# Kernel optimization log

Measured on AMD Instinct MI355X. Metric: run time of the kernel, lower is better.

The kernel has to match this reference:

```python
import jax, jax.numpy as jnp
import numpy as np

B, Q, DIM, HEADS, RPE_H, HGRID, WGRID, STRIDE = 2, 900, 256, 8, 512, 64, 64, 16
KV = HGRID * WGRID


def setup_inputs() -> dict:
    key = jax.random.key(0)
    ks = jax.random.split(key, 16)
    s = 0.02
    return {
        "hidden_states": jax.random.normal(ks[0], (B, Q, DIM), jnp.float32),
        "reference_points": jax.random.uniform(ks[1], (B, Q, 1, 4), jnp.float32),
        "key_value_states": jax.random.normal(ks[2], (B, KV, DIM), jnp.float32),
        "spatial_shapes": jnp.array([[HGRID, WGRID]], dtype=jnp.int64),
        "attention_mask": jax.random.randint(ks[3], (B, KV), 0, 2, jnp.int32),
        "mlp1_w1": jax.random.normal(ks[4], (RPE_H, 2), jnp.float32) * s,
        "mlp1_b1": jnp.zeros((RPE_H,), jnp.float32),
        "mlp1_w2": jax.random.normal(ks[5], (HEADS, RPE_H), jnp.float32) * s,
        "mlp2_w1": jax.random.normal(ks[6], (RPE_H, 2), jnp.float32) * s,
        "mlp2_b1": jnp.zeros((RPE_H,), jnp.float32),
        "mlp2_w2": jax.random.normal(ks[7], (HEADS, RPE_H), jnp.float32) * s,
        "q_w": jax.random.normal(ks[8], (DIM, DIM), jnp.float32) * s,
        "q_b": jnp.zeros((DIM,), jnp.float32),
        "k_w": jax.random.normal(ks[9], (DIM, DIM), jnp.float32) * s,
        "k_b": jnp.zeros((DIM,), jnp.float32),
        "v_w": jax.random.normal(ks[10], (DIM, DIM), jnp.float32) * s,
        "v_b": jnp.zeros((DIM,), jnp.float32),
        "o_w": jax.random.normal(ks[11], (DIM, DIM), jnp.float32) * s,
        "o_b": jnp.zeros((DIM,), jnp.float32),
    }


def _attn(hidden_states, reference_points, key_value_states, h, w, attention_mask,
          mlp1_w1, mlp1_b1, mlp1_w2, mlp2_w1, mlp2_b1, mlp2_w2,
          q_w, q_b, k_w, k_b, v_w, v_b, o_w, o_b):
    b, q_len, dim = hidden_states.shape
    nh = mlp1_w2.shape[0]
    hd = dim // nh
    scale = hd ** -0.5
    stride = STRIDE

    # boxes cxcywh -> x1y1x2y2, scaled to absolute pixel coords (reparam=False)
    c, sz = reference_points[..., :2], reference_points[..., 2:]
    ref = jnp.concatenate([c - sz / 2, c + sz / 2], axis=-1)  # (B,Q,1,4)
    mult = jnp.array([w * stride, h * stride, w * stride, h * stride], dtype=ref.dtype)
    ref = ref * mult

    pos_x = (jnp.arange(w, dtype=jnp.float32) + 0.5) * stride
    pos_y = (jnp.arange(h, dtype=jnp.float32) + 0.5) * stride
    dx = ref[..., 0::2] - pos_x[None, None, :, None]  # (B,Q,W,2)
    dy = ref[..., 1::2] - pos_y[None, None, :, None]  # (B,Q,H,2)

    # small MLPs: 2 -> rpe_hidden -> num_heads
    rpe_x = jax.nn.relu(dx @ mlp1_w1.T + mlp1_b1) @ mlp1_w2.T  # (B,Q,W,nh)
    rpe_y = jax.nn.relu(dy @ mlp2_w1.T + mlp2_b1) @ mlp2_w2.T  # (B,Q,H,nh)
    rpe = rpe_x[:, :, None, :, :] + rpe_y[:, :, :, None, :]    # (B,Q,H,W,nh)
    rpe = rpe.reshape(b, q_len, h * w, nh).transpose(0, 3, 1, 2)  # (B,nh,Q,K)

    queries = (hidden_states @ q_w.T + q_b).reshape(b, q_len, nh, hd).transpose(0, 2, 1, 3) * scale
    kv_len = key_value_states.shape[1]
    keys = (key_value_states @ k_w.T + k_b).reshape(b, kv_len, nh, hd).transpose(0, 2, 1, 3)
    values = (key_value_states @ v_w.T + v_b).reshape(b, kv_len, nh, hd).transpose(0, 2, 1, 3)

    scores = jnp.einsum('bhqd,bhkd->bhqk', queries, keys) + rpe
    scores = scores + attention_mask.astype(scores.dtype)[:, None, None] * (-100.0)
    probs = jax.nn.softmax(scores, axis=-1)
    ctx = jnp.einsum('bhqk,bhkd->bhqd', probs, values)
    ctx = ctx.transpose(0, 2, 1, 3).reshape(b, q_len, dim)
    return ctx @ o_w.T + o_b


def reference(hidden_states, reference_points, key_value_states, spatial_shapes, attention_mask,
              mlp1_w1, mlp1_b1, mlp1_w2, mlp2_w1, mlp2_b1, mlp2_w2,
              q_w, q_b, k_w, k_b, v_w, v_b, o_w, o_b):
    h = int(spatial_shapes[0, 0])
    w = int(spatial_shapes[0, 1])
    return _attn(hidden_states, reference_points, key_value_states, h, w, attention_mask,
                 mlp1_w1, mlp1_b1, mlp1_w2, mlp2_w1, mlp2_b1, mlp2_w2,
                 q_w, q_b, k_w, k_b, v_w, v_b, o_w, o_b)
```

## Files before the change

### kernel.cpp

```cpp
#include <hip/hip_runtime.h>
#include <math.h>

#define NB    2
#define NQ    900
#define NQP   960
#define NKV   4096
#define DIMM  256
#define NHEAD 8
#define HD    32
#define RPEH  512
#define GRID  64
#define SPLIT 4
#define KVSEG 1024
#define NT    16

typedef short short8 __attribute__((ext_vector_type(8)));
typedef float f32x4 __attribute__((ext_vector_type(4)));
typedef unsigned uint2v __attribute__((ext_vector_type(2)));
typedef unsigned short u16;
typedef unsigned short u16x4 __attribute__((ext_vector_type(4)));

__device__ inline u16 f2bf(float f) {
    unsigned u = __builtin_bit_cast(unsigned, f);
    u += 0x7fff + ((u >> 16) & 1);
    return (u16)(u >> 16);
}
__device__ inline unsigned packbf2(float a, float b) {
    unsigned ua = __builtin_bit_cast(unsigned, a);
    ua += 0x7fff + ((ua >> 16) & 1);
    unsigned ub = __builtin_bit_cast(unsigned, b);
    ub += 0x7fff + ((ub >> 16) & 1);
    return (ua >> 16) | (ub & 0xffff0000u);
}

#define HS4  115200
#define KV4  524288
#define W4   16384
__global__ __launch_bounds__(256) void conv_bf16(
    const float* __restrict__ hs, const float* __restrict__ kv,
    const float* __restrict__ qw, const float* __restrict__ kw,
    const float* __restrict__ vw,
    u16* __restrict__ hsbf, u16* __restrict__ kvbf,
    u16* __restrict__ qwbf, u16* __restrict__ kwbf, u16* __restrict__ vwbf)
{
    const int total = HS4 + KV4 + 3 * W4;
    for (int g = blockIdx.x * 256 + threadIdx.x; g < total; g += gridDim.x * 256) {
        const float* s; u16* d; int off;
        if (g < HS4)                       { s = hs; d = hsbf; off = g; }
        else if (g < HS4 + KV4)            { s = kv; d = kvbf; off = g - HS4; }
        else if (g < HS4 + KV4 + W4)       { s = qw; d = qwbf; off = g - HS4 - KV4; }
        else if (g < HS4 + KV4 + 2 * W4)   { s = kw; d = kwbf; off = g - HS4 - KV4 - W4; }
        else                               { s = vw; d = vwbf; off = g - HS4 - KV4 - 2 * W4; }
        f32x4 v = *(const f32x4*)(s + (size_t)off * 4);
        *(u16x4*)(d + (size_t)off * 4) =
            (u16x4){f2bf(v[0]), f2bf(v[1]), f2bf(v[2]), f2bf(v[3])};
    }
}

__global__ __launch_bounds__(256) void proj_mfma(
    const u16* __restrict__ A,
    const u16* __restrict__ W0, const float* __restrict__ B0,
    const u16* __restrict__ W1, const float* __restrict__ B1,
    u16* __restrict__ outRow, u16* __restrict__ outVt,
    int M, float scale)
{
    __shared__ u16 Abuf[2][4096];
    __shared__ u16 Bbuf[2][4096];

    const u16* W = W0; const float* bias = B0; bool vt = false;
    if (blockIdx.z == 1) { W = W1; bias = B1; vt = true; }

    const int t    = threadIdx.x;
    const int lane = t & 63;
    const int w    = t >> 6;
    const int wm   = w >> 1, wn = w & 1;
    const int m0   = blockIdx.x * 128;
    const int n0   = blockIdx.y * 128;

    const int r0 = t >> 2, c0 = t & 3;
    const int r1 = r0 + 64;
    const int s0 = r0 * 4 + (c0 ^ (r0 & 3));
    const int s1 = r1 * 4 + (c0 ^ (r1 & 3));
    const u16* Arow0 = A + (size_t)(m0 + r0) * DIMM + c0 * 8;
    const u16* Arow1 = A + (size_t)(m0 + r1) * DIMM + c0 * 8;
    const u16* Wrow0 = W + (size_t)(n0 + r0) * DIMM + c0 * 8;
    const u16* Wrow1 = W + (size_t)(n0 + r1) * DIMM + c0 * 8;

    const int fr = lane & 15, fkc = lane >> 4;
    int aslot[4], bslot[4];
    #pragma unroll
    for (int f = 0; f < 4; ++f) {
        int ar = wm * 64 + f * 16 + fr;
        int br = wn * 64 + f * 16 + fr;
        aslot[f] = ar * 4 + (fkc ^ (ar & 3));
        bslot[f] = br * 4 + (fkc ^ (br & 3));
    }
    float bv[4];
    #pragma unroll
    for (int f = 0; f < 4; ++f) bv[f] = bias[n0 + wn * 64 + f * 16 + fr];

    f32x4 acc[4][4] = {};

    {
        short8 a0 = *(const short8*)(Arow0);
        short8 a1 = *(const short8*)(Arow1);
        short8 b0 = *(const short8*)(Wrow0);
        short8 b1 = *(const short8*)(Wrow1);
        *(short8*)&Abuf[0][s0 * 8] = a0;
        *(short8*)&Abuf[0][s1 * 8] = a1;
        *(short8*)&Bbuf[0][s0 * 8] = b0;
        *(short8*)&Bbuf[0][s1 * 8] = b1;
    }
    __syncthreads();

    int cur = 0;
    for (int kt = 0; kt < 8; ++kt) {
        short8 na0, na1, nb0, nb1;
        if (kt < 7) {
            int ko = (kt + 1) * 32;
            na0 = *(const short8*)(Arow0 + ko);
            na1 = *(const short8*)(Arow1 + ko);
            nb0 = *(const short8*)(Wrow0 + ko);
            nb1 = *(const short8*)(Wrow1 + ko);
        }
        short8 af[4], bf[4];
        #pragma unroll
        for (int f = 0; f < 4; ++f) {
            af[f] = *(const short8*)&Abuf[cur][aslot[f] * 8];
            bf[f] = *(const short8*)&Bbuf[cur][bslot[f] * 8];
        }
        #pragma unroll
        for (int i = 0; i < 4; ++i)
            #pragma unroll
            for (int j = 0; j < 4; ++j)
                acc[i][j] = __builtin_amdgcn_mfma_f32_16x16x32_bf16(af[i], bf[j], acc[i][j], 0, 0, 0);
        if (kt < 7) {
            *(short8*)&Abuf[cur ^ 1][s0 * 8] = na0;
            *(short8*)&Abuf[cur ^ 1][s1 * 8] = na1;
            *(short8*)&Bbuf[cur ^ 1][s0 * 8] = nb0;
            *(short8*)&Bbuf[cur ^ 1][s1 * 8] = nb1;
        }
        __syncthreads();
        cur ^= 1;
    }

    #pragma unroll
    for (int i = 0; i < 4; ++i) {
        int mbase = m0 + wm * 64 + i * 16 + 4 * fkc;
        #pragma unroll
        for (int j = 0; j < 4; ++j) {
            int n = n0 + wn * 64 + j * 16 + fr;
            #pragma unroll
            for (int r = 0; r < 4; ++r) {
                int gm = mbase + r;
                if (gm < M) {
                    float v = (acc[i][j][r] + bv[j]) * scale;
                    if (!vt) {
                        outRow[(size_t)gm * DIMM + n] = f2bf(v);
                    } else {
                        int bb = gm >> 12, kvi = gm & 4095;
                        int hh = n >> 5, dd = n & 31;
                        outVt[(size_t)((bb * NHEAD + hh) * HD + dd) * NKV + kvi] = f2bf(v);
                    }
                }
            }
        }
    }
}

__global__ __launch_bounds__(256) void rpe_kernel(
    const float* __restrict__ ref_pts,
    const float* __restrict__ w1x, const float* __restrict__ b1x,
    const float* __restrict__ w2x,
    const float* __restrict__ w1y, const float* __restrict__ b1y,
    const float* __restrict__ w2y,
    float* __restrict__ rpex, float* __restrict__ rpey)
{
    __shared__ f32x4 wpk[RPEH];
    __shared__ float w2t[RPEH][NHEAD];
    __shared__ float2 red[3][4][4][64];

    const int t   = threadIdx.x;
    const int m   = blockIdx.x & 1;
    const int bq0 = (blockIdx.x >> 1) * 4;

    const float* w1 = m ? w1y : w1x;
    const float* b1 = m ? b1y : b1x;
    const float* w2 = m ? w2y : w2x;
    for (int r = t; r < RPEH; r += 256) {
        float a = w1[r * 2], b = w1[r * 2 + 1];
        wpk[r] = (f32x4){a, b, b1[r], a + b};
    }
    for (int i = t; i < RPEH * NHEAD; i += 256) {
        int h = i >> 9, r = i & 511;
        w2t[r][h] = w2[h * RPEH + r];
    }
    __syncthreads();

    const int lane = t & 63;
    const int wv   = t >> 6;
    const float p  = (lane + 0.5f) * 16.f;

    float lo[4], hi[4];
    #pragma unroll
    for (int j = 0; j < 4; ++j) {
        const float* q = ref_pts + (size_t)(bq0 + j) * 4;
        float c = m ? q[1] : q[0];
        float s = m ? q[3] : q[2];
        lo[j] = (c - s * 0.5f) * 1024.f;
        hi[j] = (c + s * 0.5f) * 1024.f;
    }

    float2 acc[4][4] = {};
    const int r0 = wv * 128;
    #pragma unroll 4
    for (int rr = 0; rr < 128; ++rr) {
        int r = r0 + rr;
        f32x4 W  = wpk[r];
        f32x4 u0 = *(const f32x4*)&w2t[r][0];
        f32x4 u1 = *(const f32x4*)&w2t[r][4];
        float bp = W[3] * p;
        #pragma unroll
        for (int tk = 0; tk < 4; ++tk) {
            float al  = W[0] * lo[tk] + W[1] * hi[tk] + W[2];
            float hid = fmaxf(al - bp, 0.f);
            acc[tk][0].x += u0[0] * hid;  acc[tk][0].y += u0[1] * hid;
            acc[tk][1].x += u0[2] * hid;  acc[tk][1].y += u0[3] * hid;
            acc[tk][2].x += u1[0] * hid;  acc[tk][2].y += u1[1] * hid;
            acc[tk][3].x += u1[2] * hid;  acc[tk][3].y += u1[3] * hid;
        }
    }

    if (wv > 0) {
        #pragma unroll
        for (int tk = 0; tk < 4; ++tk)
            #pragma unroll
            for (int j = 0; j < 4; ++j)
                red[wv - 1][tk][j][lane] = acc[tk][j];
    }
    __syncthreads();
    if (wv == 0) {
        float* outp = m ? rpey : rpex;
        #pragma unroll
        for (int tk = 0; tk < 4; ++tk) {
            size_t base = (size_t)(bq0 + tk) * (NHEAD * GRID) + lane;
            #pragma unroll
            for (int j = 0; j < 4; ++j) {
                float2 s0 = red[0][tk][j][lane];
                float2 s1 = red[1][tk][j][lane];
                float2 s2 = red[2][tk][j][lane];
                float sx = acc[tk][j].x + s0.x + s1.x + s2.x;
                float sy = acc[tk][j].y + s0.y + s1.y + s2.y;
                outp[base + (2 * j) * GRID]     = sx;
                outp[base + (2 * j + 1) * GRID] = sy;
            }
        }
    }
}

__global__ __launch_bounds__(256) void attn_mfma(
    const u16* __restrict__ Qbf, const u16* __restrict__ Kbf,
    const u16* __restrict__ Vt,
    const float* __restrict__ RX, const float* __restrict__ RY,
    const int* __restrict__ mask,
    float* __restrict__ pctx, float2* __restrict__ pml)
{
    __shared__ short8 kbuf[2][4][64];
    __shared__ short8 vbuf[2][4][64];
    __shared__ unsigned pbuf[4][2][64][4];
    __shared__ float ry_s[16][68];
    __shared__ float mbuf[2][64];

    const int tid  = threadIdx.x;
    const int lane = tid & 63;
    const int w    = tid >> 6;
    const int q15  = lane & 15;
    const int g    = lane >> 4;
    const int qt = blockIdx.x, h = blockIdx.y;
    const int b  = blockIdx.z >> 2;
    const int sp = blockIdx.z & 3;
    const int q0 = qt * 64;
    const int wq = w * 16 + q15;
    const int gq = q0 + wq;
    const bool qok = gq < NQ;
    const int kv0g = sp * KVSEG;

    float rxr[16];
    {
        const float* rxrow = RX + (size_t)(b * NQ + (qok ? gq : 0)) * (NHEAD * GRID) + h * GRID;
        #pragma unroll
        for (int kt = 0; kt < 4; ++kt)
            #pragma unroll
            for (int r = 0; r < 4; ++r)
                rxr[kt * 4 + r] = qok ? rxrow[16 * kt + 4 * g + r] : 0.f;
    }
    for (int idx = tid; idx < 16 * 64; idx += 256) {
        int y = idx & 15, q = idx >> 4;
        int gq2 = q0 + q;
        ry_s[y][q] = (gq2 < NQ)
            ? RY[(size_t)(b * NQ + gq2) * (NHEAD * GRID) + h * GRID + sp * 16 + y] : 0.f;
    }

    short8 qf = *(const short8*)(Qbf + ((size_t)(b * NQ + gq)) * DIMM + h * HD + 8 * g);

    const int sr = tid >> 2, sc = tid & 3;
    const int vd = tid >> 3, vc = tid & 7;
    const size_t kbase = ((size_t)(b * NKV + kv0g + sr)) * DIMM + h * HD + 8 * sc;
    const size_t vbase = ((size_t)((b * NHEAD + h) * HD + vd)) * NKV + kv0g + 8 * vc;

    kbuf[0][sr >> 4][(sr & 15) + 16 * sc] = *(const short8*)(Kbf + kbase);
    vbuf[0][(vc >> 2) * 2 + (vd >> 4)][16 * (vc & 3) + (vd & 15)] = *(const short8*)(Vt + vbase);
    if (tid < 64) mbuf[0][tid] = -100.f * (float)mask[b * NKV + kv0g + tid];
    __syncthreads();

    f32x4 cacc0 = {0.f, 0.f, 0.f, 0.f};
    f32x4 cacc1 = {0.f, 0.f, 0.f, 0.f};
    float m_run = -1e30f, l_run = 0.f;
    int cur = 0;

    for (int t = 0; t < NT; ++t) {
        short8 rk = {}, rv = {};
        float rm = 0.f;
        if (t < NT - 1) {
            size_t kvn = (size_t)(t + 1) * 64;
            rk = *(const short8*)(Kbf + kbase + kvn * DIMM);
            rv = *(const short8*)(Vt + vbase + kvn);
            if (tid < 64) rm = -100.f * (float)mask[b * NKV + kv0g + kvn + tid];
        }

        f32x4 zero = {0.f, 0.f, 0.f, 0.f};
        f32x4 s[4];
        __builtin_amdgcn_s_setprio(1);
        #pragma unroll
        for (int kt = 0; kt < 4; ++kt)
            s[kt] = __builtin_amdgcn_mfma_f32_16x16x32_bf16(kbuf[cur][kt][lane], qf, zero, 0, 0, 0);
        __builtin_amdgcn_s_setprio(0);

        float ryb = ry_s[t][wq];
        #pragma unroll
        for (int kt = 0; kt < 4; ++kt) {
            #pragma unroll
            for (int r = 0; r < 4; ++r)
                s[kt][r] += rxr[kt * 4 + r] + ryb + mbuf[cur][16 * kt + 4 * g + r];
        }

        float mloc = s[0][0];
        #pragma unroll
        for (int kt = 0; kt < 4; ++kt)
            #pragma unroll
            for (int r = 0; r < 4; ++r) mloc = fmaxf(mloc, s[kt][r]);
        mloc = fmaxf(mloc, __shfl_xor(mloc, 16));
        mloc = fmaxf(mloc, __shfl_xor(mloc, 32));
        float mnew = fmaxf(m_run, mloc);
        float fsc  = __expf(m_run - mnew);
        float psum = 0.f;
        #pragma unroll
        for (int kt = 0; kt < 4; ++kt)
            #pragma unroll
            for (int r = 0; r < 4; ++r) {
                float pv = __expf(s[kt][r] - mnew);
                s[kt][r] = pv;
                psum += pv;
            }
        psum += __shfl_xor(psum, 16);
        psum += __shfl_xor(psum, 32);
        l_run = l_run * fsc + psum;
        m_run = mnew;
        cacc0 *= fsc;
        cacc1 *= fsc;

        #pragma unroll
        for (int kt = 0; kt < 4; ++kt) {
            unsigned d0 = packbf2(s[kt][0], s[kt][1]);
            unsigned d1 = packbf2(s[kt][2], s[kt][3]);
            int lt = 16 * ((2 * kt + (g >> 1)) & 3) + q15;
            uint2v* dst = (uint2v*)&pbuf[w][kt >> 1][lt][2 * (g & 1)];
            *dst = (uint2v){d0, d1};
        }

        __builtin_amdgcn_s_setprio(1);
        #pragma unroll
        for (int sk = 0; sk < 2; ++sk) {
            short8 pf = *(const short8*)&pbuf[w][sk][lane][0];
            cacc0 = __builtin_amdgcn_mfma_f32_16x16x32_bf16(vbuf[cur][sk * 2 + 0][lane], pf, cacc0, 0, 0, 0);
            cacc1 = __builtin_amdgcn_mfma_f32_16x16x32_bf16(vbuf[cur][sk * 2 + 1][lane], pf, cacc1, 0, 0, 0);
        }
        __builtin_amdgcn_s_setprio(0);

        if (t < NT - 1) {
            kbuf[cur ^ 1][sr >> 4][(sr & 15) + 16 * sc] = rk;
            vbuf[cur ^ 1][(vc >> 2) * 2 + (vd >> 4)][16 * (vc & 3) + (vd & 15)] = rv;
            if (tid < 64) mbuf[cur ^ 1][tid] = rm;
        }
        __syncthreads();
        cur ^= 1;
    }

    size_t prow = (size_t)(sp * NB + b) * NQP + gq;
    float* pc = pctx + prow * DIMM + h * HD;
    #pragma unroll
    for (int r = 0; r < 4; ++r) {
        pc[4 * g + r]      = cacc0[r];
        pc[16 + 4 * g + r] = cacc1[r];
    }
    if (g == 0) {
        float2 v; v.x = m_run; v.y = l_run;
        pml[prow * NHEAD + h] = v;
    }
}

__global__ __launch_bounds__(256) void attn_reduce(
    const float* __restrict__ pctx, const float2* __restrict__ pml,
    float* __restrict__ CTX)
{
    const int bq = blockIdx.x;
    const int b = bq / NQ, q = bq - b * NQ;
    const int c = threadIdx.x;
    const int h = c >> 5;

    float m[SPLIT], l[SPLIT];
    #pragma unroll
    for (int sp = 0; sp < SPLIT; ++sp) {
        float2 v = pml[((size_t)(sp * NB + b) * NQP + q) * NHEAD + h];
        m[sp] = v.x; l[sp] = v.y;
    }
    float ms = fmaxf(fmaxf(m[0], m[1]), fmaxf(m[2], m[3]));
    float L = 0.f, acc = 0.f;
    #pragma unroll
    for (int sp = 0; sp < SPLIT; ++sp) {
        float wgt = __expf(m[sp] - ms);
        L   += wgt * l[sp];
        acc += wgt * pctx[((size_t)(sp * NB + b) * NQP + q) * DIMM + c];
    }
    CTX[(size_t)bq * DIMM + c] = acc / L;
}

__global__ __launch_bounds__(256) void gemm_bias_f32(
    const float* __restrict__ A, const float* __restrict__ W,
    const float* __restrict__ bias, float* __restrict__ C,
    int M, int N, int K)
{
    __shared__ float As[32][33];
    __shared__ float Ws[32][33];
    const int t  = threadIdx.x;
    const int tr = t >> 4;
    const int tc = t & 15;
    const int brow = blockIdx.y * 32;
    const int bcol = blockIdx.x * 32;
    float acc00 = 0.f, acc01 = 0.f, acc10 = 0.f, acc11 = 0.f;

    for (int kt = 0; kt < K; kt += 32) {
        #pragma unroll
        for (int i = 0; i < 4; ++i) {
            int idx = t + i * 256;
            int r = idx >> 5, c = idx & 31;
            int gr = brow + r;
            As[r][c] = (gr < M) ? A[(size_t)gr * K + kt + c] : 0.f;
            Ws[r][c] = W[(size_t)(bcol + r) * K + kt + c];
        }
        __syncthreads();
        #pragma unroll 8
        for (int k = 0; k < 32; ++k) {
            float a0 = As[tr * 2][k], a1 = As[tr * 2 + 1][k];
            float w0 = Ws[tc * 2][k], w1 = Ws[tc * 2 + 1][k];
            acc00 += a0 * w0; acc01 += a0 * w1;
            acc10 += a1 * w0; acc11 += a1 * w1;
        }
        __syncthreads();
    }
    int gc0 = bcol + tc * 2, gc1 = gc0 + 1;
    int gr0 = brow + tr * 2, gr1 = gr0 + 1;
    if (gr0 < M) {
        C[(size_t)gr0 * N + gc0] = acc00 + bias[gc0];
        C[(size_t)gr0 * N + gc1] = acc01 + bias[gc1];
    }
    if (gr1 < M) {
        C[(size_t)gr1 * N + gc0] = acc10 + bias[gc0];
        C[(size_t)gr1 * N + gc1] = acc11 + bias[gc1];
    }
}

extern "C" void kernel_launch(void* const* d_in, const int* in_sizes, int n_in,
                              void* d_out, int out_size, void* d_ws, size_t ws_size,
                              hipStream_t stream)
{
    const float* hs   = (const float*)d_in[0];
    const float* rp   = (const float*)d_in[1];
    const float* kv   = (const float*)d_in[2];
    const int*   msk  = (const int*)d_in[4];
    const float* m1w1 = (const float*)d_in[5];
    const float* m1b1 = (const float*)d_in[6];
    const float* m1w2 = (const float*)d_in[7];
    const float* m2w1 = (const float*)d_in[8];
    const float* m2b1 = (const float*)d_in[9];
    const float* m2w2 = (const float*)d_in[10];
    const float* q_w  = (const float*)d_in[11];
    const float* q_b  = (const float*)d_in[12];
    const float* k_w  = (const float*)d_in[13];
    const float* k_b  = (const float*)d_in[14];
    const float* v_w  = (const float*)d_in[15];
    const float* v_b  = (const float*)d_in[16];
    const float* o_w  = (const float*)d_in[17];
    const float* o_b  = (const float*)d_in[18];
    float* out = (float*)d_out;

    char* p = (char*)d_ws;
    float* RX   = (float*)p; p += (size_t)NB * NQ * NHEAD * GRID * 4;
    float* RY   = (float*)p; p += (size_t)NB * NQ * NHEAD * GRID * 4;
    float* CTX  = (float*)p; p += (size_t)NB * NQ * DIMM * 4;
    u16*   Qbf  = (u16*)p;   p += (size_t)1920 * DIMM * 2;
    u16*   Kbf  = (u16*)p;   p += (size_t)NB * NKV * DIMM * 2;
    u16*   Vt   = (u16*)p;   p += (size_t)NB * NHEAD * HD * NKV * 2;

    char* u = p;
    u16* hsbf = (u16*)u;
    u16* kvbf = hsbf + (size_t)1920 * DIMM;
    u16* qwbf = kvbf + (size_t)NB * NKV * DIMM;
    u16* kwbf = qwbf + (size_t)DIMM * DIMM;
    u16* vwbf = kwbf + (size_t)DIMM * DIMM;
    float*  pctx = (float*)u;
    float2* pml  = (float2*)(pctx + (size_t)SPLIT * NB * NQP * DIMM);

    const float scale = 0.17677669529663687f;

    conv_bf16<<<1024, 256, 0, stream>>>(hs, kv, q_w, k_w, v_w,
                                        hsbf, kvbf, qwbf, kwbf, vwbf);

    proj_mfma<<<dim3(15, 2, 1), 256, 0, stream>>>(
        hsbf, qwbf, q_b, nullptr, nullptr, Qbf, nullptr, NB * NQ, scale);

    proj_mfma<<<dim3(64, 2, 2), 256, 0, stream>>>(
        kvbf, kwbf, k_b, vwbf, v_b, Kbf, Vt, NB * NKV, 1.f);

    rpe_kernel<<<900, 256, 0, stream>>>(rp, m1w1, m1b1, m1w2,
                                        m2w1, m2b1, m2w2, RX, RY);

    attn_mfma<<<dim3((NQ + 63) / 64, NHEAD, NB * SPLIT), 256, 0, stream>>>(
        Qbf, Kbf, Vt, RX, RY, msk, pctx, pml);

    attn_reduce<<<NB * NQ, 256, 0, stream>>>(pctx, pml, CTX);

    gemm_bias_f32<<<dim3(DIMM / 32, (NB * NQ + 31) / 32), 256, 0, stream>>>(
        CTX, o_w, o_b, out, NB * NQ, DIMM, DIMM);
}
```

Before: 141.8 us.

## Split KV eight ways, fold log2e into scores, interleave P packing with MFMA

Templates the split-KV attention and reduce kernels on the split count and uses eight KV segments when the workspace is large enough, which doubles the block count to fill more compute units. It folds log2(e) into the query scale, the RPE second-layer weights and the mask bias so softmax can use exp2f directly. It also shrinks the P staging buffer by packing each half just before its MFMA, and uses a tree max. The extra split doubles the partial-context traffic and the work in the reduce kernel, and the chosen path depends on the workspace size.

```diff
diff --git a/kernel.cpp b/kernel.cpp
--- a/kernel.cpp
+++ b/kernel.cpp
@@ -10,9 +10,8 @@
 #define HD    32
 #define RPEH  512
 #define GRID  64
-#define SPLIT 4
-#define KVSEG 1024
-#define NT    16
+
+#define LOG2E 1.4426950408889634f
 
 typedef short short8 __attribute__((ext_vector_type(8)));
 typedef float f32x4 __attribute__((ext_vector_type(4)));
@@ -193,7 +192,7 @@
     }
     for (int i = t; i < RPEH * NHEAD; i += 256) {
         int h = i >> 9, r = i & 511;
-        w2t[r][h] = w2[h * RPEH + r];
+        w2t[r][h] = w2[h * RPEH + r] * LOG2E;
     }
     __syncthreads();
 
@@ -258,6 +257,7 @@
     }
 }
 
+template <int SPL>
 __global__ __launch_bounds__(256) void attn_mfma(
     const u16* __restrict__ Qbf, const u16* __restrict__ Kbf,
     const u16* __restrict__ Vt,
@@ -265,10 +265,12 @@
     const int* __restrict__ mask,
     float* __restrict__ pctx, float2* __restrict__ pml)
 {
+    constexpr int KSEG = NKV / SPL;
+    constexpr int NTS  = KSEG / 64;
     __shared__ short8 kbuf[2][4][64];
     __shared__ short8 vbuf[2][4][64];
-    __shared__ unsigned pbuf[4][2][64][4];
-    __shared__ float ry_s[16][68];
+    __shared__ unsigned pbuf[4][64][4];
+    __shared__ float ry_s[NTS][68];
     __shared__ float mbuf[2][64];
 
     const int tid  = threadIdx.x;
@@ -277,13 +279,13 @@
     const int q15  = lane & 15;
     const int g    = lane >> 4;
     const int qt = blockIdx.x, h = blockIdx.y;
-    const int b  = blockIdx.z >> 2;
-    const int sp = blockIdx.z & 3;
+    const int b  = blockIdx.z / SPL;
+    const int sp = blockIdx.z % SPL;
     const int q0 = qt * 64;
     const int wq = w * 16 + q15;
     const int gq = q0 + wq;
     const bool qok = gq < NQ;
-    const int kv0g = sp * KVSEG;
+    const int kv0g = sp * KSEG;
 
     float rxr[16];
     {
@@ -294,11 +296,11 @@
             for (int r = 0; r < 4; ++r)
                 rxr[kt * 4 + r] = qok ? rxrow[16 * kt + 4 * g + r] : 0.f;
     }
-    for (int idx = tid; idx < 16 * 64; idx += 256) {
-        int y = idx & 15, q = idx >> 4;
+    for (int idx = tid; idx < NTS * 64; idx += 256) {
+        int y = idx % NTS, q = idx / NTS;
         int gq2 = q0 + q;
         ry_s[y][q] = (gq2 < NQ)
-            ? RY[(size_t)(b * NQ + gq2) * (NHEAD * GRID) + h * GRID + sp * 16 + y] : 0.f;
+            ? RY[(size_t)(b * NQ + gq2) * (NHEAD * GRID) + h * GRID + sp * NTS + y] : 0.f;
     }
 
     short8 qf = *(const short8*)(Qbf + ((size_t)(b * NQ + gq)) * DIMM + h * HD + 8 * g);
@@ -310,7 +312,7 @@
 
     kbuf[0][sr >> 4][(sr & 15) + 16 * sc] = *(const short8*)(Kbf + kbase);
     vbuf[0][(vc >> 2) * 2 + (vd >> 4)][16 * (vc & 3) + (vd & 15)] = *(const short8*)(Vt + vbase);
-    if (tid < 64) mbuf[0][tid] = -100.f * (float)mask[b * NKV + kv0g + tid];
+    if (tid < 64) mbuf[0][tid] = -(100.f * LOG2E) * (float)mask[b * NKV + kv0g + tid];
     __syncthreads();
 
     f32x4 cacc0 = {0.f, 0.f, 0.f, 0.f};
@@ -318,14 +320,14 @@
     float m_run = -1e30f, l_run = 0.f;
     int cur = 0;
 
-    for (int t = 0; t < NT; ++t) {
+    for (int t = 0; t < NTS; ++t) {
         short8 rk = {}, rv = {};
         float rm = 0.f;
-        if (t < NT - 1) {
+        if (t < NTS - 1) {
             size_t kvn = (size_t)(t + 1) * 64;
             rk = *(const short8*)(Kbf + kbase + kvn * DIMM);
             rv = *(const short8*)(Vt + vbase + kvn);
-            if (tid < 64) rm = -100.f * (float)mask[b * NKV + kv0g + kvn + tid];
+            if (tid < 64) rm = -(100.f * LOG2E) * (float)mask[b * NKV + kv0g + kvn + tid];
         }
 
         f32x4 zero = {0.f, 0.f, 0.f, 0.f};
@@ -344,21 +346,21 @@
                 s[kt][r] += rxr[kt * 4 + r] + ryb + mbuf[cur][16 * kt + 4 * g + r];
         }
 
-        float mloc = s[0][0];
+        float mk[4];
         #pragma unroll
         for (int kt = 0; kt < 4; ++kt)
-            #pragma unroll
-            for (int r = 0; r < 4; ++r) mloc = fmaxf(mloc, s[kt][r]);
+            mk[kt] = fmaxf(fmaxf(s[kt][0], s[kt][1]), fmaxf(s[kt][2], s[kt][3]));
+        float mloc = fmaxf(fmaxf(mk[0], mk[1]), fmaxf(mk[2], mk[3]));
         mloc = fmaxf(mloc, __shfl_xor(mloc, 16));
         mloc = fmaxf(mloc, __shfl_xor(mloc, 32));
         float mnew = fmaxf(m_run, mloc);
-        float fsc  = __expf(m_run - mnew);
+        float fsc  = exp2f(m_run - mnew);
         float psum = 0.f;
         #pragma unroll
         for (int kt = 0; kt < 4; ++kt)
             #pragma unroll
             for (int r = 0; r < 4; ++r) {
-                float pv = __expf(s[kt][r] - mnew);
+                float pv = exp2f(s[kt][r] - mnew);
                 s[kt][r] = pv;
                 psum += pv;
             }
@@ -369,25 +371,25 @@
         cacc0 *= fsc;
         cacc1 *= fsc;
 
-        #pragma unroll
-        for (int kt = 0; kt < 4; ++kt) {
-            unsigned d0 = packbf2(s[kt][0], s[kt][1]);
-            unsigned d1 = packbf2(s[kt][2], s[kt][3]);
-            int lt = 16 * ((2 * kt + (g >> 1)) & 3) + q15;
-            uint2v* dst = (uint2v*)&pbuf[w][kt >> 1][lt][2 * (g & 1)];
-            *dst = (uint2v){d0, d1};
-        }
-
         __builtin_amdgcn_s_setprio(1);
         #pragma unroll
         for (int sk = 0; sk < 2; ++sk) {
-            short8 pf = *(const short8*)&pbuf[w][sk][lane][0];
+            #pragma unroll
+            for (int kk = 0; kk < 2; ++kk) {
+                int kt = sk * 2 + kk;
+                unsigned d0 = packbf2(s[kt][0], s[kt][1]);
+                unsigned d1 = packbf2(s[kt][2], s[kt][3]);
+                int lt = 16 * ((2 * kt + (g >> 1)) & 3) + q15;
+                uint2v* dst = (uint2v*)&pbuf[w][lt][2 * (g & 1)];
+                *dst = (uint2v){d0, d1};
+            }
+            short8 pf = *(const short8*)&pbuf[w][lane][0];
             cacc0 = __builtin_amdgcn_mfma_f32_16x16x32_bf16(vbuf[cur][sk * 2 + 0][lane], pf, cacc0, 0, 0, 0);
             cacc1 = __builtin_amdgcn_mfma_f32_16x16x32_bf16(vbuf[cur][sk * 2 + 1][lane], pf, cacc1, 0, 0, 0);
         }
         __builtin_amdgcn_s_setprio(0);
 
-        if (t < NT - 1) {
+        if (t < NTS - 1) {
             kbuf[cur ^ 1][sr >> 4][(sr & 15) + 16 * sc] = rk;
             vbuf[cur ^ 1][(vc >> 2) * 2 + (vd >> 4)][16 * (vc & 3) + (vd & 15)] = rv;
             if (tid < 64) mbuf[cur ^ 1][tid] = rm;
@@ -409,6 +411,7 @@
     }
 }
 
+template <int SPL>
 __global__ __launch_bounds__(256) void attn_reduce(
     const float* __restrict__ pctx, const float2* __restrict__ pml,
     float* __restrict__ CTX)
@@ -418,17 +421,19 @@
     const int c = threadIdx.x;
     const int h = c >> 5;
 
-    float m[SPLIT], l[SPLIT];
-    #pragma unroll
-    for (int sp = 0; sp < SPLIT; ++sp) {
+    float m[SPL], l[SPL];
+    #pragma unroll
+    for (int sp = 0; sp < SPL; ++sp) {
         float2 v = pml[((size_t)(sp * NB + b) * NQP + q) * NHEAD + h];
         m[sp] = v.x; l[sp] = v.y;
     }
-    float ms = fmaxf(fmaxf(m[0], m[1]), fmaxf(m[2], m[3]));
+    float ms = m[0];
+    #pragma unroll
+    for (int sp = 1; sp < SPL; ++sp) ms = fmaxf(ms, m[sp]);
     float L = 0.f, acc = 0.f;
     #pragma unroll
-    for (int sp = 0; sp < SPLIT; ++sp) {
-        float wgt = __expf(m[sp] - ms);
+    for (int sp = 0; sp < SPL; ++sp) {
+        float wgt = exp2f(m[sp] - ms);
         L   += wgt * l[sp];
         acc += wgt * pctx[((size_t)(sp * NB + b) * NQP + q) * DIMM + c];
     }
@@ -518,10 +523,15 @@
     u16* qwbf = kvbf + (size_t)NB * NKV * DIMM;
     u16* kwbf = qwbf + (size_t)DIMM * DIMM;
     u16* vwbf = kwbf + (size_t)DIMM * DIMM;
-    float*  pctx = (float*)u;
-    float2* pml  = (float2*)(pctx + (size_t)SPLIT * NB * NQP * DIMM);
-
-    const float scale = 0.17677669529663687f;
+    float* pctx = (float*)u;
+
+    const size_t fixed_bytes = (size_t)(u - (char*)d_ws);
+    const size_t need8 = fixed_bytes
+                       + (size_t)8 * NB * NQP * DIMM * 4
+                       + (size_t)8 * NB * NQP * NHEAD * sizeof(float2);
+    const bool use8 = (ws_size >= need8);
+
+    const float scale = 0.17677669529663687f * LOG2E;
 
     conv_bf16<<<1024, 256, 0, stream>>>(hs, kv, q_w, k_w, v_w,
                                         hsbf, kvbf, qwbf, kwbf, vwbf);
@@ -535,10 +545,17 @@
     rpe_kernel<<<900, 256, 0, stream>>>(rp, m1w1, m1b1, m1w2,
                                         m2w1, m2b1, m2w2, RX, RY);
 
-    attn_mfma<<<dim3((NQ + 63) / 64, NHEAD, NB * SPLIT), 256, 0, stream>>>(
-        Qbf, Kbf, Vt, RX, RY, msk, pctx, pml);
-
-    attn_reduce<<<NB * NQ, 256, 0, stream>>>(pctx, pml, CTX);
+    if (use8) {
+        float2* pml = (float2*)(pctx + (size_t)8 * NB * NQP * DIMM);
+        attn_mfma<8><<<dim3((NQ + 63) / 64, NHEAD, NB * 8), 256, 0, stream>>>(
+            Qbf, Kbf, Vt, RX, RY, msk, pctx, pml);
+        attn_reduce<8><<<NB * NQ, 256, 0, stream>>>(pctx, pml, CTX);
+    } else {
+        float2* pml = (float2*)(pctx + (size_t)4 * NB * NQP * DIMM);
+        attn_mfma<4><<<dim3((NQ + 63) / 64, NHEAD, NB * 4), 256, 0, stream>>>(
+            Qbf, Kbf, Vt, RX, RY, msk, pctx, pml);
+        attn_reduce<4><<<NB * NQ, 256, 0, stream>>>(pctx, pml, CTX);
+    }
 
     gemm_bias_f32<<<dim3(DIMM / 32, (NB * NQ + 31) / 32), 256, 0, stream>>>(
         CTX, o_w, o_b, out, NB * NQ, DIMM, DIMM);
```

New measurement: 149.0 us, median of 2. +5.1%, slower.
